# Performance work log

Hardware: AMD Instinct MI355X
Metric: run time of the kernel (lower is better)

Reference implementation:

```python
import jax, jax.numpy as jnp
import numpy as np

B, S, D, MEM, STRIDE = 8, 8192, 128, 128, 64

def setup_inputs() -> dict:
    key = jax.random.key(0)
    ks = jax.random.split(key, 6)
    scale = 0.01  # matches nn.init.normal_(w, 0.0, 0.01)
    x = jax.random.normal(ks[0], (B, S, D), dtype=jnp.float32)
    Wq = scale * jax.random.normal(ks[1], (D, D), dtype=jnp.float32)
    Wk = scale * jax.random.normal(ks[2], (D, D), dtype=jnp.float32)
    Wv = scale * jax.random.normal(ks[3], (MEM, D), dtype=jnp.float32)
    Wg_w = jnp.zeros((1, D), dtype=jnp.float32)       # W_g weight init zeros
    Wg_b = jnp.full((1,), -2.0, dtype=jnp.float32)    # W_g bias init -2.0
    Wout = scale * jax.random.normal(ks[4], (D, MEM), dtype=jnp.float32)
    return {"x": x, "Wq": Wq, "Wk": Wk, "Wv": Wv, "Wg_w": Wg_w, "Wg_b": Wg_b, "Wout": Wout}

def reference(x, Wq, Wk, Wv, Wg_w, Wg_b, Wout):
    b, s, d = x.shape
    nC = s // STRIDE  # S assumed divisible by stride
    q = x @ Wq.T                                  # [B,S,D]
    k = x @ Wk.T                                  # [B,S,D]
    v = x @ Wv.T                                  # [B,S,MEM]
    g = jax.nn.sigmoid(x @ Wg_w.T + Wg_b)         # [B,S,1]
    # chunk: leading scan axis nC
    qc = q.reshape(b, nC, STRIDE, d).transpose(1, 0, 2, 3)
    kc = k.reshape(b, nC, STRIDE, d).transpose(1, 0, 2, 3)
    vc = v.reshape(b, nC, STRIDE, MEM).transpose(1, 0, 2, 3)
    gc = g.reshape(b, nC, STRIDE, 1).transpose(1, 0, 2, 3)

    def step(M, chunk):
        qch, kch, vch, gch = chunk
        reads = jnp.einsum('bsd,bdm->bsm', qch, M)              # read before write
        write = jnp.einsum('bsd,bsm->bdm', kch * gch, vch)      # gated outer-product
        avg_gate = gch.mean(axis=1, keepdims=True)              # [B,1,1]
        M_new = (1.0 - avg_gate) * M + write
        return M_new, reads

    M0 = jnp.zeros((b, d, MEM), dtype=x.dtype)
    _, reads = jax.lax.scan(step, M0, (qc, kc, vc, gc))         # [nC,B,STRIDE,MEM]
    out = reads.transpose(1, 0, 2, 3).reshape(b, s, MEM)
    return out @ Wout.T                                         # [B,S,D]
```

## Files before the change

### kernel.cpp

```cpp
#include <hip/hip_runtime.h>

#define Bn 8
#define Sn 8192
#define Dn 128
#define NCn 128

typedef _Float16 f16;
typedef f16 f16x2 __attribute__((ext_vector_type(2)));
typedef f16 f16x4 __attribute__((ext_vector_type(4)));
typedef float f32x4 __attribute__((ext_vector_type(4)));

static __device__ __forceinline__ f32x4 mfma16(f16x4 a, f16x4 b, f32x4 c) {
  return __builtin_amdgcn_mfma_f32_16x16x16f16(a, b, c, 0, 0, 0);
}

union UU { uint4 u; f16x2 h[4]; f16x4 q[2]; };


__global__ __launch_bounds__(256) void k_prep(
    const float* __restrict__ Wq, const float* __restrict__ Wk,
    const float* __restrict__ Wv, const float* __restrict__ Wout,
    f16* __restrict__ Amat, f16* __restrict__ r2) {
  const int blk = blockIdx.x;
  const int which = blk >> 4;
  const int w = threadIdx.x >> 6;
  const int t = (blk & 15) * 4 + w;
  const int ti = t >> 3, tj = t & 7;
  const int lane = threadIdx.x & 63, r16 = lane & 15, g4 = lane >> 4;
  f32x4 acc = {};
  if (which == 0) {
#pragma unroll
    for (int kk = 0; kk < 8; ++kk) {
      f16x4 af, bf;
#pragma unroll
      for (int j = 0; j < 4; ++j) {
        af[j] = (f16)Wq[(kk * 16 + g4 * 4 + j) * 128 + ti * 16 + r16];
        bf[j] = (f16)Wk[(kk * 16 + g4 * 4 + j) * 128 + tj * 16 + r16];
      }
      acc = mfma16(af, bf, acc);
    }
  } else {
#pragma unroll
    for (int kk = 0; kk < 8; ++kk) {
      f16x4 af, bf;
      float4 a4 = *(const float4*)(Wout + (ti * 16 + r16) * 128 + kk * 16 + g4 * 4);
      af[0] = (f16)a4.x; af[1] = (f16)a4.y; af[2] = (f16)a4.z; af[3] = (f16)a4.w;
#pragma unroll
      for (int j = 0; j < 4; ++j)
        bf[j] = (f16)Wv[(kk * 16 + g4 * 4 + j) * 128 + tj * 16 + r16];
      acc = mfma16(af, bf, acc);
    }
  }
  f16* dst = which ? r2 : Amat;
#pragma unroll
  for (int j = 0; j < 4; ++j)
    dst[(ti * 16 + g4 * 4 + j) * 128 + tj * 16 + r16] = (f16)acc[j];
}

__global__ __launch_bounds__(512, 8) void k_phase1(
    const float* __restrict__ x, const float* __restrict__ gw, const float* __restrict__ gb,
    const f16* __restrict__ Amat, const f16* __restrict__ r2,
    f16x4* __restrict__ wtg, float* __restrict__ gavg, f16* __restrict__ xh) {
  __shared__ __align__(16) f16 Xs[64][136];
  __shared__ __align__(16) f16x4 vP[2048];
  __shared__ float gs[64];
  const int h = blockIdx.x;
  const int b = h & 7, seg = (h >> 3) & 15, m = h >> 7;
  const int c = seg * 8 + m;
  const int tid = threadIdx.x;
  {
    int s = tid >> 3, sub = tid & 7;
    const float* xrow = x + ((size_t)b * Sn + (size_t)c * 64 + s) * Dn;
    f16* xhrow = xh + (size_t)(b * NCn + c) * 8192 + s * 128;
    float gpart = 0.f;
#pragma unroll
    for (int i = 0; i < 4; ++i) {
      int col = sub * 4 + i * 32;
      float4 v = *(const float4*)(xrow + col);
      float4 g = *(const float4*)(gw + col);
      gpart += v.x * g.x + v.y * g.y + v.z * g.z + v.w * g.w;
      f16x4 hh = {(f16)v.x, (f16)v.y, (f16)v.z, (f16)v.w};
      *(f16x4*)&Xs[s][col] = hh;
      *(f16x4*)&xhrow[col] = hh;
    }
    gpart += __shfl_xor(gpart, 1);
    gpart += __shfl_xor(gpart, 2);
    gpart += __shfl_xor(gpart, 4);
    if (sub == 0) gs[s] = 1.f / (1.f + __expf(-(gpart + gb[0])));
  }
  __syncthreads();
  if (tid == 0) {
    float sum = 0.f;
#pragma unroll
    for (int i = 0; i < 64; ++i) sum += gs[i];
    gavg[b * NCn + c] = sum * (1.f / 64.f);
  }
  const int w = tid >> 6, lane = tid & 63, r16 = lane & 15, g4 = lane >> 4;
  f32x4 uacc[4] = {}, vacc[4] = {};
#pragma unroll
  for (int kk = 0; kk < 8; ++kk) {
    f16x4 bu = *(const f16x4*)&Amat[(w * 16 + r16) * 128 + kk * 16 + g4 * 4];
    f16x4 bv = *(const f16x4*)&r2[(w * 16 + r16) * 128 + kk * 16 + g4 * 4];
#pragma unroll
    for (int mr = 0; mr < 4; ++mr) {
      f16x4 af = *(f16x4*)&Xs[mr * 16 + r16][kk * 16 + g4 * 4];
      uacc[mr] = mfma16(af, bu, uacc[mr]);
      vacc[mr] = mfma16(af, bv, vacc[mr]);
    }
  }
  f16x4 ua[4];
#pragma unroll
  for (int mr = 0; mr < 4; ++mr) {
    float g0 = gs[mr * 16 + g4 * 4 + 0], g1 = gs[mr * 16 + g4 * 4 + 1];
    float g2 = gs[mr * 16 + g4 * 4 + 2], g3 = gs[mr * 16 + g4 * 4 + 3];
    f16x4 uh = {(f16)(uacc[mr][0] * g0), (f16)(uacc[mr][1] * g1),
                (f16)(uacc[mr][2] * g2), (f16)(uacc[mr][3] * g3)};
    ua[mr] = uh;
    f16x4 vh = {(f16)vacc[mr][0], (f16)vacc[mr][1], (f16)vacc[mr][2], (f16)vacc[mr][3]};
    vP[(mr * 8 + w) * 64 + lane] = vh;
  }
  __syncthreads();
  f32x4 z[8] = {};
#pragma unroll
  for (int ks = 0; ks < 4; ++ks)
#pragma unroll
    for (int ct = 0; ct < 8; ++ct)
      z[ct] = mfma16(ua[ks], vP[(ks * 8 + ct) * 64 + lane], z[ct]);
  f16x4* wdst = wtg + (size_t)(b * NCn + c) * 4096;
#pragma unroll
  for (int ct = 0; ct < 8; ++ct) {
    f16x4 zh = {(f16)z[ct][0], (f16)z[ct][1], (f16)z[ct][2], (f16)z[ct][3]};
    wdst[(w * 8 + ct) * 64 + lane] = zh;
  }
}

__global__ __launch_bounds__(512, 4) void k_outfold(
    const f16* __restrict__ xh, const uint4* __restrict__ wtg4,
    const float* __restrict__ gavg, float* __restrict__ outp) {
  __shared__ __align__(16) f16 Xs[2][64][136];
  __shared__ __align__(16) f16x4 Mh4[2][1024];
  const int blk = blockIdx.x;
  const int b = blk & 7, q = (blk >> 3) & 3, seg = 15 - (blk >> 5);
  const int tid = threadIdx.x;
  const int w = tid >> 6, lane = tid & 63, r16 = lane & 15, g4 = lane >> 4;
  const int mr = w & 3, tq = w >> 2;
  const int lt = tid >> 5;
  const int gtile = (lt >> 1) * 8 + q * 2 + (lt & 1);
  const int slot = tid & 31;

  float4 M0 = {0.f, 0.f, 0.f, 0.f}, M1 = {0.f, 0.f, 0.f, 0.f};
  {
    const uint4* Zb = wtg4 + (size_t)(b * NCn) * 2048 + gtile * 32 + slot;
    const float* ga = gavg + b * NCn;
    const int nt = seg * 8;
#pragma unroll 8
    for (int t = 0; t < nt; ++t) {
      UU z; z.u = Zb[(size_t)t * 2048];
      float dd = 1.f - ga[t];
      M0.x = dd * M0.x + (float)z.h[0][0];
      M0.y = dd * M0.y + (float)z.h[0][1];
      M0.z = dd * M0.z + (float)z.h[1][0];
      M0.w = dd * M0.w + (float)z.h[1][1];
      M1.x = dd * M1.x + (float)z.h[2][0];
      M1.y = dd * M1.y + (float)z.h[2][1];
      M1.z = dd * M1.z + (float)z.h[3][0];
      M1.w = dd * M1.w + (float)z.h[3][1];
    }
  }

  float dseg[8];
#pragma unroll
  for (int t = 0; t < 8; ++t) dseg[t] = 1.f - gavg[b * NCn + seg * 8 + t];

  const uint4* Zseg = wtg4 + (size_t)(b * NCn + seg * 8) * 2048;
  const f16* xhseg = xh + (size_t)(b * NCn + seg * 8) * 8192;
  const int xrow = tid >> 3, xcol = (tid & 7) * 16;

  uint4 xa = ((const uint4*)xhseg)[tid * 2];
  uint4 xb2 = ((const uint4*)xhseg)[tid * 2 + 1];

#pragma unroll
  for (int m = 0; m < 8; ++m) {
    f16(*Xsb)[136] = Xs[m & 1];
    f16x4* Mh = Mh4[m & 1];
    *(uint4*)&Xsb[xrow][xcol] = xa;
    *(uint4*)&Xsb[xrow][xcol + 8] = xb2;
    Mh[tid * 2] = (f16x4){(f16)M0.x, (f16)M0.y, (f16)M0.z, (f16)M0.w};
    Mh[tid * 2 + 1] = (f16x4){(f16)M1.x, (f16)M1.y, (f16)M1.z, (f16)M1.w};
    __syncthreads();

    UU z;
    z.u = Zseg[(size_t)m * 2048 + gtile * 32 + slot];
    if (m < 7) {
      const uint4* xn = (const uint4*)(xhseg + (size_t)(m + 1) * 8192);
      xa = xn[tid * 2];
      xb2 = xn[tid * 2 + 1];
    }

    f32x4 acc = {};
#pragma unroll
    for (int kk = 0; kk < 8; ++kk) {
      f16x4 af = *(f16x4*)&Xsb[mr * 16 + r16][kk * 16 + g4 * 4];
      f16x4 bf = Mh[(kk * 2 + tq) * 64 + lane];
      acc = mfma16(af, bf, acc);
    }

    {
      float dd = dseg[m];
      M0.x = dd * M0.x + (float)z.h[0][0];
      M0.y = dd * M0.y + (float)z.h[0][1];
      M0.z = dd * M0.z + (float)z.h[1][0];
      M0.w = dd * M0.w + (float)z.h[1][1];
      M1.x = dd * M1.x + (float)z.h[2][0];
      M1.y = dd * M1.y + (float)z.h[2][1];
      M1.z = dd * M1.z + (float)z.h[3][0];
      M1.w = dd * M1.w + (float)z.h[3][1];
    }

    {
      const int c = seg * 8 + m;
      float* ob = outp + ((size_t)b * Sn + (size_t)c * 64 + mr * 16 + g4 * 4) * Dn +
                  (q * 2 + tq) * 16 + r16;
#pragma unroll
      for (int j = 0; j < 4; ++j) ob[(size_t)j * Dn] = acc[j];
    }
  }
}

extern "C" void kernel_launch(void* const* d_in, const int* in_sizes, int n_in,
                              void* d_out, int out_size, void* d_ws, size_t ws_size,
                              hipStream_t stream) {
  const float* x = (const float*)d_in[0];
  const float* Wq = (const float*)d_in[1];
  const float* Wk = (const float*)d_in[2];
  const float* Wv = (const float*)d_in[3];
  const float* gw = (const float*)d_in[4];
  const float* gb = (const float*)d_in[5];
  const float* Wout = (const float*)d_in[6];

  char* ws = (char*)d_ws;
  f16* Amat = (f16*)(ws + 0);
  f16* r2 = (f16*)(ws + 32768);
  float* gavg = (float*)(ws + 65536);
  f16* wtg = (f16*)(ws + 69632);
  f16* xh = (f16*)(ws + 37556224);

  k_prep<<<dim3(32), dim3(256), 0, stream>>>(Wq, Wk, Wv, Wout, Amat, r2);
  k_phase1<<<dim3(Bn * NCn), dim3(512), 0, stream>>>(x, gw, gb, Amat, r2, (f16x4*)wtg,
                                                     gavg, xh);
  k_outfold<<<dim3(512), dim3(512), 0, stream>>>(xh, (const uint4*)wtg, gavg,
                                                 (float*)d_out);
}
```

Measured before the change: 57.89 us.

## Compute per-segment local memory states in phase1 and combine with decayed prefix

After: 75.62 us. 30.6% more time.

```diff
diff --git a/kernel.cpp b/kernel.cpp
--- a/kernel.cpp
+++ b/kernel.cpp
@@ -57,114 +57,142 @@
     dst[(ti * 16 + g4 * 4 + j) * 128 + tj * 16 + r16] = (f16)acc[j];
 }
 
-__global__ __launch_bounds__(512, 8) void k_phase1(
+__global__ __launch_bounds__(512, 2) void k_phase1seg(
     const float* __restrict__ x, const float* __restrict__ gw, const float* __restrict__ gb,
     const f16* __restrict__ Amat, const f16* __restrict__ r2,
-    f16x4* __restrict__ wtg, float* __restrict__ gavg, f16* __restrict__ xh) {
+    f16x4* __restrict__ Sbuf, float* __restrict__ gavg, f16* __restrict__ xh,
+    float4* __restrict__ Lf) {
   __shared__ __align__(16) f16 Xs[64][136];
   __shared__ __align__(16) f16x4 vP[2048];
   __shared__ float gs[64];
-  const int h = blockIdx.x;
-  const int b = h & 7, seg = (h >> 3) & 15, m = h >> 7;
-  const int c = seg * 8 + m;
+  const int blk = blockIdx.x;
+  const int b = blk & 7, seg = blk >> 3;
   const int tid = threadIdx.x;
+  const int w = tid >> 6, lane = tid & 63, r16 = lane & 15, g4 = lane >> 4;
+  const int s = tid >> 3, sub = tid & 7;
+
+  float4 gwr[4], xr[4];
+#pragma unroll
+  for (int i = 0; i < 4; ++i) gwr[i] = *(const float4*)(gw + sub * 4 + i * 32);
   {
-    int s = tid >> 3, sub = tid & 7;
-    const float* xrow = x + ((size_t)b * Sn + (size_t)c * 64 + s) * Dn;
-    f16* xhrow = xh + (size_t)(b * NCn + c) * 8192 + s * 128;
-    float gpart = 0.f;
-#pragma unroll
-    for (int i = 0; i < 4; ++i) {
-      int col = sub * 4 + i * 32;
-      float4 v = *(const float4*)(xrow + col);
-      float4 g = *(const float4*)(gw + col);
-      gpart += v.x * g.x + v.y * g.y + v.z * g.z + v.w * g.w;
-      f16x4 hh = {(f16)v.x, (f16)v.y, (f16)v.z, (f16)v.w};
-      *(f16x4*)&Xs[s][col] = hh;
-      *(f16x4*)&xhrow[col] = hh;
-    }
-    gpart += __shfl_xor(gpart, 1);
-    gpart += __shfl_xor(gpart, 2);
-    gpart += __shfl_xor(gpart, 4);
-    if (sub == 0) gs[s] = 1.f / (1.f + __expf(-(gpart + gb[0])));
-  }
-  __syncthreads();
-  if (tid == 0) {
-    float sum = 0.f;
-#pragma unroll
-    for (int i = 0; i < 64; ++i) sum += gs[i];
-    gavg[b * NCn + c] = sum * (1.f / 64.f);
-  }
-  const int w = tid >> 6, lane = tid & 63, r16 = lane & 15, g4 = lane >> 4;
-  f32x4 uacc[4] = {}, vacc[4] = {};
-#pragma unroll
-  for (int kk = 0; kk < 8; ++kk) {
-    f16x4 bu = *(const f16x4*)&Amat[(w * 16 + r16) * 128 + kk * 16 + g4 * 4];
-    f16x4 bv = *(const f16x4*)&r2[(w * 16 + r16) * 128 + kk * 16 + g4 * 4];
+    const float* xrow = x + ((size_t)b * Sn + (size_t)seg * 512 + s) * Dn;
+#pragma unroll
+    for (int i = 0; i < 4; ++i) xr[i] = *(const float4*)(xrow + sub * 4 + i * 32);
+  }
+
+  f32x4 Sreg[8] = {};
+  const float gbias = gb[0];
+
+#pragma unroll
+  for (int m = 0; m < 8; ++m) {
+    const int c = seg * 8 + m;
+    {
+      f16* xhrow = xh + (size_t)(b * NCn + c) * 8192 + s * 128;
+      float gpart = 0.f;
+#pragma unroll
+      for (int i = 0; i < 4; ++i) {
+        int col = sub * 4 + i * 32;
+        float4 v = xr[i];
+        gpart += v.x * gwr[i].x + v.y * gwr[i].y + v.z * gwr[i].z + v.w * gwr[i].w;
+        f16x4 hh = {(f16)v.x, (f16)v.y, (f16)v.z, (f16)v.w};
+        *(f16x4*)&Xs[s][col] = hh;
+        *(f16x4*)&xhrow[col] = hh;
+      }
+      gpart += __shfl_xor(gpart, 1);
+      gpart += __shfl_xor(gpart, 2);
+      gpart += __shfl_xor(gpart, 4);
+      if (sub == 0) gs[s] = 1.f / (1.f + __expf(-(gpart + gbias)));
+    }
+    __syncthreads();
+
+    if (m < 7) {
+      const float* xn = x + ((size_t)b * Sn + (size_t)(c + 1) * 64 + s) * Dn;
+#pragma unroll
+      for (int i = 0; i < 4; ++i) xr[i] = *(const float4*)(xn + sub * 4 + i * 32);
+    }
+
+    float gsum = 0.f;
+#pragma unroll
+    for (int i = 0; i < 64; ++i) gsum += gs[i];
+    const float dc = 1.f - gsum * (1.f / 64.f);
+    if (tid == 0) gavg[b * NCn + c] = gsum * (1.f / 64.f);
+
+    f32x4 uacc[4] = {}, vacc[4] = {};
+#pragma unroll
+    for (int kk = 0; kk < 8; ++kk) {
+      f16x4 bu = *(const f16x4*)&Amat[(w * 16 + r16) * 128 + kk * 16 + g4 * 4];
+      f16x4 bv = *(const f16x4*)&r2[(w * 16 + r16) * 128 + kk * 16 + g4 * 4];
+#pragma unroll
+      for (int mr = 0; mr < 4; ++mr) {
+        f16x4 af = *(f16x4*)&Xs[mr * 16 + r16][kk * 16 + g4 * 4];
+        uacc[mr] = mfma16(af, bu, uacc[mr]);
+        vacc[mr] = mfma16(af, bv, vacc[mr]);
+      }
+    }
+    f16x4 ua[4];
 #pragma unroll
     for (int mr = 0; mr < 4; ++mr) {
-      f16x4 af = *(f16x4*)&Xs[mr * 16 + r16][kk * 16 + g4 * 4];
-      uacc[mr] = mfma16(af, bu, uacc[mr]);
-      vacc[mr] = mfma16(af, bv, vacc[mr]);
-    }
-  }
-  f16x4 ua[4];
-#pragma unroll
-  for (int mr = 0; mr < 4; ++mr) {
-    float g0 = gs[mr * 16 + g4 * 4 + 0], g1 = gs[mr * 16 + g4 * 4 + 1];
-    float g2 = gs[mr * 16 + g4 * 4 + 2], g3 = gs[mr * 16 + g4 * 4 + 3];
-    f16x4 uh = {(f16)(uacc[mr][0] * g0), (f16)(uacc[mr][1] * g1),
-                (f16)(uacc[mr][2] * g2), (f16)(uacc[mr][3] * g3)};
-    ua[mr] = uh;
-    f16x4 vh = {(f16)vacc[mr][0], (f16)vacc[mr][1], (f16)vacc[mr][2], (f16)vacc[mr][3]};
-    vP[(mr * 8 + w) * 64 + lane] = vh;
-  }
-  __syncthreads();
-  f32x4 z[8] = {};
-#pragma unroll
-  for (int ks = 0; ks < 4; ++ks)
-#pragma unroll
-    for (int ct = 0; ct < 8; ++ct)
-      z[ct] = mfma16(ua[ks], vP[(ks * 8 + ct) * 64 + lane], z[ct]);
-  f16x4* wdst = wtg + (size_t)(b * NCn + c) * 4096;
+      float g0 = gs[mr * 16 + g4 * 4 + 0], g1 = gs[mr * 16 + g4 * 4 + 1];
+      float g2 = gs[mr * 16 + g4 * 4 + 2], g3 = gs[mr * 16 + g4 * 4 + 3];
+      f16x4 uh = {(f16)(uacc[mr][0] * g0), (f16)(uacc[mr][1] * g1),
+                  (f16)(uacc[mr][2] * g2), (f16)(uacc[mr][3] * g3)};
+      ua[mr] = uh;
+      f16x4 vh = {(f16)vacc[mr][0], (f16)vacc[mr][1], (f16)vacc[mr][2], (f16)vacc[mr][3]};
+      vP[(mr * 8 + w) * 64 + lane] = vh;
+    }
+    __syncthreads();
+
+    f32x4 z[8] = {};
+#pragma unroll
+    for (int ks = 0; ks < 4; ++ks)
+#pragma unroll
+      for (int ct = 0; ct < 8; ++ct)
+        z[ct] = mfma16(ua[ks], vP[(ks * 8 + ct) * 64 + lane], z[ct]);
+    f16x4* wdst = Sbuf + (size_t)(b * NCn + c) * 4096;
+#pragma unroll
+    for (int ct = 0; ct < 8; ++ct) {
+      f16x4 sh = {(f16)Sreg[ct][0], (f16)Sreg[ct][1], (f16)Sreg[ct][2], (f16)Sreg[ct][3]};
+      wdst[(w * 8 + ct) * 64 + lane] = sh;
+#pragma unroll
+      for (int j = 0; j < 4; ++j) Sreg[ct][j] = dc * Sreg[ct][j] + z[ct][j];
+    }
+  }
+  float4* lfd = Lf + (size_t)(b * 16 + seg) * 4096;
 #pragma unroll
   for (int ct = 0; ct < 8; ++ct) {
-    f16x4 zh = {(f16)z[ct][0], (f16)z[ct][1], (f16)z[ct][2], (f16)z[ct][3]};
-    wdst[(w * 8 + ct) * 64 + lane] = zh;
-  }
-}
-
-__global__ __launch_bounds__(512, 4) void k_outfold(
-    const f16* __restrict__ xh, const uint4* __restrict__ wtg4,
-    const float* __restrict__ gavg, float* __restrict__ outp) {
+    float4 o = {Sreg[ct][0], Sreg[ct][1], Sreg[ct][2], Sreg[ct][3]};
+    lfd[(w * 8 + ct) * 64 + lane] = o;
+  }
+}
+
+__global__ __launch_bounds__(512, 4) void k_outfold2(
+    const f16* __restrict__ xh, const uint4* __restrict__ Sbuf4,
+    const float4* __restrict__ Lf, const float* __restrict__ gavg,
+    float* __restrict__ outp) {
   __shared__ __align__(16) f16 Xs[2][64][136];
   __shared__ __align__(16) f16x4 Mh4[2][1024];
   const int blk = blockIdx.x;
-  const int b = blk & 7, q = (blk >> 3) & 3, seg = 15 - (blk >> 5);
+  const int b = blk & 7, q = (blk >> 3) & 3, seg = blk >> 5;
   const int tid = threadIdx.x;
   const int w = tid >> 6, lane = tid & 63, r16 = lane & 15, g4 = lane >> 4;
   const int mr = w & 3, tq = w >> 2;
   const int lt = tid >> 5;
   const int gtile = (lt >> 1) * 8 + q * 2 + (lt & 1);
   const int slot = tid & 31;
-
-  float4 M0 = {0.f, 0.f, 0.f, 0.f}, M1 = {0.f, 0.f, 0.f, 0.f};
+  const int f4i = gtile * 64 + slot * 2;
+
+  float4 P0 = {0.f, 0.f, 0.f, 0.f}, P1 = {0.f, 0.f, 0.f, 0.f};
   {
-    const uint4* Zb = wtg4 + (size_t)(b * NCn) * 2048 + gtile * 32 + slot;
-    const float* ga = gavg + b * NCn;
-    const int nt = seg * 8;
-#pragma unroll 8
-    for (int t = 0; t < nt; ++t) {
-      UU z; z.u = Zb[(size_t)t * 2048];
-      float dd = 1.f - ga[t];
-      M0.x = dd * M0.x + (float)z.h[0][0];
-      M0.y = dd * M0.y + (float)z.h[0][1];
-      M0.z = dd * M0.z + (float)z.h[1][0];
-      M0.w = dd * M0.w + (float)z.h[1][1];
-      M1.x = dd * M1.x + (float)z.h[2][0];
-      M1.y = dd * M1.y + (float)z.h[2][1];
-      M1.z = dd * M1.z + (float)z.h[3][0];
-      M1.w = dd * M1.w + (float)z.h[3][1];
+    float wgt = 1.f;
+    for (int t = seg - 1; t >= 0; --t) {
+      const float4* lp = Lf + (size_t)(b * 16 + t) * 4096;
+      float4 a = lp[f4i], c4 = lp[f4i + 1];
+      P0.x += wgt * a.x; P0.y += wgt * a.y; P0.z += wgt * a.z; P0.w += wgt * a.w;
+      P1.x += wgt * c4.x; P1.y += wgt * c4.y; P1.z += wgt * c4.z; P1.w += wgt * c4.w;
+      float df = 1.f;
+#pragma unroll
+      for (int i = 0; i < 8; ++i) df *= (1.f - gavg[b * NCn + t * 8 + i]);
+      wgt *= df;
     }
   }
 
@@ -172,30 +200,38 @@
 #pragma unroll
   for (int t = 0; t < 8; ++t) dseg[t] = 1.f - gavg[b * NCn + seg * 8 + t];
 
-  const uint4* Zseg = wtg4 + (size_t)(b * NCn + seg * 8) * 2048;
+  const uint4* Sseg = Sbuf4 + (size_t)(b * NCn + seg * 8) * 2048;
   const f16* xhseg = xh + (size_t)(b * NCn + seg * 8) * 8192;
   const int xrow = tid >> 3, xcol = (tid & 7) * 16;
 
   uint4 xa = ((const uint4*)xhseg)[tid * 2];
   uint4 xb2 = ((const uint4*)xhseg)[tid * 2 + 1];
-
+  UU sv; sv.u = Sseg[gtile * 32 + slot];
+
+  float pf = 1.f;
 #pragma unroll
   for (int m = 0; m < 8; ++m) {
     f16(*Xsb)[136] = Xs[m & 1];
     f16x4* Mh = Mh4[m & 1];
     *(uint4*)&Xsb[xrow][xcol] = xa;
     *(uint4*)&Xsb[xrow][xcol + 8] = xb2;
-    Mh[tid * 2] = (f16x4){(f16)M0.x, (f16)M0.y, (f16)M0.z, (f16)M0.w};
-    Mh[tid * 2 + 1] = (f16x4){(f16)M1.x, (f16)M1.y, (f16)M1.z, (f16)M1.w};
+    Mh[tid * 2] = (f16x4){(f16)((float)sv.h[0][0] + pf * P0.x),
+                          (f16)((float)sv.h[0][1] + pf * P0.y),
+                          (f16)((float)sv.h[1][0] + pf * P0.z),
+                          (f16)((float)sv.h[1][1] + pf * P0.w)};
+    Mh[tid * 2 + 1] = (f16x4){(f16)((float)sv.h[2][0] + pf * P1.x),
+                              (f16)((float)sv.h[2][1] + pf * P1.y),
+                              (f16)((float)sv.h[3][0] + pf * P1.z),
+                              (f16)((float)sv.h[3][1] + pf * P1.w)};
     __syncthreads();
 
-    UU z;
-    z.u = Zseg[(size_t)m * 2048 + gtile * 32 + slot];
     if (m < 7) {
       const uint4* xn = (const uint4*)(xhseg + (size_t)(m + 1) * 8192);
       xa = xn[tid * 2];
       xb2 = xn[tid * 2 + 1];
-    }
+      sv.u = Sseg[(size_t)(m + 1) * 2048 + gtile * 32 + slot];
+    }
+    pf *= dseg[m];
 
     f32x4 acc = {};
 #pragma unroll
@@ -203,18 +239,6 @@
       f16x4 af = *(f16x4*)&Xsb[mr * 16 + r16][kk * 16 + g4 * 4];
       f16x4 bf = Mh[(kk * 2 + tq) * 64 + lane];
       acc = mfma16(af, bf, acc);
-    }
-
-    {
-      float dd = dseg[m];
-      M0.x = dd * M0.x + (float)z.h[0][0];
-      M0.y = dd * M0.y + (float)z.h[0][1];
-      M0.z = dd * M0.z + (float)z.h[1][0];
-      M0.w = dd * M0.w + (float)z.h[1][1];
-      M1.x = dd * M1.x + (float)z.h[2][0];
-      M1.y = dd * M1.y + (float)z.h[2][1];
-      M1.z = dd * M1.z + (float)z.h[3][0];
-      M1.w = dd * M1.w + (float)z.h[3][1];
     }
 
     {
@@ -242,12 +266,13 @@
   f16* Amat = (f16*)(ws + 0);
   f16* r2 = (f16*)(ws + 32768);
   float* gavg = (float*)(ws + 65536);
-  f16* wtg = (f16*)(ws + 69632);
+  f16* Sbuf = (f16*)(ws + 69632);
   f16* xh = (f16*)(ws + 37556224);
+  float4* Lf = (float4*)(ws + 54333440);
 
   k_prep<<<dim3(32), dim3(256), 0, stream>>>(Wq, Wk, Wv, Wout, Amat, r2);
-  k_phase1<<<dim3(Bn * NCn), dim3(512), 0, stream>>>(x, gw, gb, Amat, r2, (f16x4*)wtg,
-                                                     gavg, xh);
-  k_outfold<<<dim3(512), dim3(512), 0, stream>>>(xh, (const uint4*)wtg, gavg,
-                                                 (float*)d_out);
-}
+  k_phase1seg<<<dim3(128), dim3(512), 0, stream>>>(x, gw, gb, Amat, r2, (f16x4*)Sbuf,
+                                                   gavg, xh, Lf);
+  k_outfold2<<<dim3(512), dim3(512), 0, stream>>>(xh, (const uint4*)Sbuf, Lf, gavg,
+                                                  (float*)d_out);
+}
```

## Precompute per-segment decayed write sums to shorten state prefix scan

Applied to the files above, without the earlier changes.

Result: faster. 56.10 us (median of 2 runs) (-3.1%).

```diff
diff --git a/kernel.cpp b/kernel.cpp
--- a/kernel.cpp
+++ b/kernel.cpp
@@ -134,13 +134,51 @@
   }
 }
 
+__global__ __launch_bounds__(512) void k_segsum(
+    const uint4* __restrict__ wtg4, const float* __restrict__ gavg,
+    float4* __restrict__ Lf) {
+  const int blk = blockIdx.x;
+  const int b = blk & 7, q = (blk >> 3) & 3, seg = blk >> 5;
+  const int tid = threadIdx.x;
+  const int lt = tid >> 5;
+  const int gtile = (lt >> 1) * 8 + q * 2 + (lt & 1);
+  const int slot = tid & 31;
+
+  float wt[8];
+  wt[7] = 1.f;
+#pragma unroll
+  for (int t = 6; t >= 0; --t)
+    wt[t] = wt[t + 1] * (1.f - gavg[b * NCn + seg * 8 + t + 1]);
+
+  const uint4* Zseg = wtg4 + (size_t)(b * NCn + seg * 8) * 2048 + gtile * 32 + slot;
+  float4 A0 = {0.f, 0.f, 0.f, 0.f}, A1 = {0.f, 0.f, 0.f, 0.f};
+#pragma unroll
+  for (int t = 0; t < 8; ++t) {
+    UU z; z.u = Zseg[(size_t)t * 2048];
+    float w = wt[t];
+    A0.x += w * (float)z.h[0][0];
+    A0.y += w * (float)z.h[0][1];
+    A0.z += w * (float)z.h[1][0];
+    A0.w += w * (float)z.h[1][1];
+    A1.x += w * (float)z.h[2][0];
+    A1.y += w * (float)z.h[2][1];
+    A1.z += w * (float)z.h[3][0];
+    A1.w += w * (float)z.h[3][1];
+  }
+  float4* lfd = Lf + (size_t)(b * 16 + seg) * 4096;
+  const int f4i = gtile * 64 + slot * 2;
+  lfd[f4i] = A0;
+  lfd[f4i + 1] = A1;
+}
+
 __global__ __launch_bounds__(512, 4) void k_outfold(
     const f16* __restrict__ xh, const uint4* __restrict__ wtg4,
-    const float* __restrict__ gavg, float* __restrict__ outp) {
+    const float4* __restrict__ Lf, const float* __restrict__ gavg,
+    float* __restrict__ outp) {
   __shared__ __align__(16) f16 Xs[2][64][136];
   __shared__ __align__(16) f16x4 Mh4[2][1024];
   const int blk = blockIdx.x;
-  const int b = blk & 7, q = (blk >> 3) & 3, seg = 15 - (blk >> 5);
+  const int b = blk & 7, q = (blk >> 3) & 3, seg = blk >> 5;
   const int tid = threadIdx.x;
   const int w = tid >> 6, lane = tid & 63, r16 = lane & 15, g4 = lane >> 4;
   const int mr = w & 3, tq = w >> 2;
@@ -150,21 +188,17 @@
 
   float4 M0 = {0.f, 0.f, 0.f, 0.f}, M1 = {0.f, 0.f, 0.f, 0.f};
   {
-    const uint4* Zb = wtg4 + (size_t)(b * NCn) * 2048 + gtile * 32 + slot;
-    const float* ga = gavg + b * NCn;
-    const int nt = seg * 8;
-#pragma unroll 8
-    for (int t = 0; t < nt; ++t) {
-      UU z; z.u = Zb[(size_t)t * 2048];
-      float dd = 1.f - ga[t];
-      M0.x = dd * M0.x + (float)z.h[0][0];
-      M0.y = dd * M0.y + (float)z.h[0][1];
-      M0.z = dd * M0.z + (float)z.h[1][0];
-      M0.w = dd * M0.w + (float)z.h[1][1];
-      M1.x = dd * M1.x + (float)z.h[2][0];
-      M1.y = dd * M1.y + (float)z.h[2][1];
-      M1.z = dd * M1.z + (float)z.h[3][0];
-      M1.w = dd * M1.w + (float)z.h[3][1];
+    const int f4i = gtile * 64 + slot * 2;
+    float wgt = 1.f;
+    for (int t = seg - 1; t >= 0; --t) {
+      const float4* lp = Lf + (size_t)(b * 16 + t) * 4096;
+      float4 a = lp[f4i], c4 = lp[f4i + 1];
+      M0.x += wgt * a.x; M0.y += wgt * a.y; M0.z += wgt * a.z; M0.w += wgt * a.w;
+      M1.x += wgt * c4.x; M1.y += wgt * c4.y; M1.z += wgt * c4.z; M1.w += wgt * c4.w;
+      float df = 1.f;
+#pragma unroll
+      for (int i = 0; i < 8; ++i) df *= (1.f - gavg[b * NCn + t * 8 + i]);
+      wgt *= df;
     }
   }
 
@@ -244,10 +278,12 @@
   float* gavg = (float*)(ws + 65536);
   f16* wtg = (f16*)(ws + 69632);
   f16* xh = (f16*)(ws + 37556224);
+  float4* Lf = (float4*)(ws + 54333440);
 
   k_prep<<<dim3(32), dim3(256), 0, stream>>>(Wq, Wk, Wv, Wout, Amat, r2);
   k_phase1<<<dim3(Bn * NCn), dim3(512), 0, stream>>>(x, gw, gb, Amat, r2, (f16x4*)wtg,
                                                      gavg, xh);
-  k_outfold<<<dim3(512), dim3(512), 0, stream>>>(xh, (const uint4*)wtg, gavg,
+  k_segsum<<<dim3(512), dim3(512), 0, stream>>>((const uint4*)wtg, gavg, Lf);
+  k_outfold<<<dim3(512), dim3(512), 0, stream>>>(xh, (const uint4*)wtg, Lf, gavg,
                                                  (float*)d_out);
 }
```
